# Kernel tuning notes

Measured on AMD Instinct MI355X. Metric: run time of the kernel, lower is better.

## Reference

```python
import jax, jax.numpy as jnp
import numpy as np

ALPHA = 0.8
TOPK = 9
LOW_BOUND = 0.0
EPS = 1e-10
IOU_EPS = 1e-6


def pairwise_iou(boxes1, boxes2):
    # boxes1 [N,4], boxes2 [G,4] in x1,y1,x2,y2 -> IoU [N,G] (mmdet BboxOverlaps2D)
    area1 = (boxes1[:, 2] - boxes1[:, 0]) * (boxes1[:, 3] - boxes1[:, 1])  # [N]
    area2 = (boxes2[:, 2] - boxes2[:, 0]) * (boxes2[:, 3] - boxes2[:, 1])  # [G]
    lt = jnp.maximum(boxes1[:, None, :2], boxes2[None, :, :2])  # [N,G,2]
    rb = jnp.minimum(boxes1[:, None, 2:], boxes2[None, :, 2:])  # [N,G,2]
    wh = jnp.clip(rb - lt, 0.0)
    inter = wh[..., 0] * wh[..., 1]  # [N,G]
    union = area1[:, None] + area2[None, :] - inter
    return inter / jnp.maximum(union, IOU_EPS)


def setup_inputs() -> dict:
    key = jax.random.key(0)
    k1, k2, k3, k4, k5, k6, k7 = jax.random.split(key, 7)
    N, G, C = 65536, 256, 80
    IMG = 1024.0
    points = jax.random.uniform(k1, (N, 2), dtype=jnp.float32) * IMG  # (cy, cx)
    p_xy1 = jax.random.uniform(k2, (N, 2), dtype=jnp.float32) * (IMG - 96.0)
    p_wh = jax.random.uniform(k3, (N, 2), dtype=jnp.float32) * 95.0 + 1.0
    bbox_preds = jnp.concatenate([p_xy1, p_xy1 + p_wh], axis=1)  # valid x1y1x2y2
    g_xy1 = jax.random.uniform(k4, (G, 2), dtype=jnp.float32) * (IMG - 256.0)
    g_wh = jax.random.uniform(k5, (G, 2), dtype=jnp.float32) * 255.0 + 1.0
    gt_bboxes = jnp.concatenate([g_xy1, g_xy1 + g_wh], axis=1)
    cls_scores = jax.random.normal(k6, (N, C), dtype=jnp.float32)
    gt_labels = jax.random.randint(k7, (G,), 0, C)
    return {"points": points, "cls_scores": cls_scores, "bbox_preds": bbox_preds,
            "gt_bboxes": gt_bboxes, "gt_labels": gt_labels}


def reference(points, cls_scores, bbox_preds, gt_bboxes, gt_labels):
    num_points = points.shape[0]
    num_gt = gt_bboxes.shape[0]
    overlaps = pairwise_iou(bbox_preds, gt_bboxes)  # [N,G]
    cls_cost = jax.nn.sigmoid(cls_scores[:, gt_labels])  # [N,G]
    overlaps = cls_cost ** (1.0 - ALPHA) * overlaps ** ALPHA
    # top-k points per GT (torch: overlaps.topk(k, dim=0))
    _, topk_idxs = jax.lax.top_k(overlaps.T, TOPK)  # [G,K]
    candidate_idxs = topk_idxs.T  # [K,G]
    cp = jnp.transpose(points[candidate_idxs], (1, 0, 2))  # [G,K,2] (cy,cx)
    # mle_2d_gaussian_2: per-GT MLE Gaussian over candidate points
    miu = cp.mean(axis=1, keepdims=True)  # [G,1,2]
    diff = cp - miu  # [G,K,2]
    sigma = jnp.einsum('gki,gkj->gij', diff, diff) / TOPK  # [G,2,2]
    a, b = sigma[:, 0, 0], sigma[:, 0, 1]
    c, d = sigma[:, 1, 0], sigma[:, 1, 1]
    det = a * d - b * c  # [G]
    inv = jnp.stack([jnp.stack([d, -b], axis=-1),
                     jnp.stack([-c, a], axis=-1)], axis=-2) / (det + EPS)[:, None, None]
    maha = jnp.einsum('gki,gij,gkj->gk', diff, inv, diff)  # [G,K]
    candidate_w = jnp.exp(-0.5 * maha).T  # [K,G]
    # center-inside-gt validity, evaluated only at candidate points
    cy, cx = cp[:, :, 0], cp[:, :, 1]  # [G,K]
    gx1, gy1, gx2, gy2 = (gt_bboxes[:, i][:, None] for i in range(4))  # [G,1]
    valid = ((cx - gx1 > EPS) & (cy - gy1 > EPS) &
             (gx2 - cx > EPS) & (gy2 - cy > EPS)).T  # [K,G]
    wv = candidate_w * valid.astype(candidate_w.dtype)
    # scatter per-GT weights to points, then max over GTs == scatter-max
    w = jnp.zeros((num_points,), dtype=cls_scores.dtype)
    w = w.at[candidate_idxs.reshape(-1)].max(wv.reshape(-1))
    w = jnp.where(w < LOW_BOUND, jnp.zeros_like(w), w)
    return w
```

## Files before the change

### kernel.cpp

```cpp
#include <hip/hip_runtime.h>
#include <hip/hip_bf16.h>
#include <math.h>

#define NPTS   65536
#define NGT    256
#define NCLS   80
#define TOPK   9
#define GSLICE 32
#define NPB    256
#define SCAP   64


__device__ inline unsigned long long pack_key(float L, unsigned idx) {
    unsigned u   = __float_as_uint(L);
    unsigned k32 = (u & 0x80000000u) ? ~u : (u | 0x80000000u);
    return ((unsigned long long)k32 << 32) | (unsigned)(~idx);
}

__global__ void zero_kernel(float* __restrict__ w, unsigned* __restrict__ cnt) {
    int i = blockIdx.x * 256 + threadIdx.x;
    if (i < NPTS) w[i] = 0.0f;
    if (i < NGT)  cnt[i] = 0u;
}

__global__ __launch_bounds__(256) void filter_kernel(
    const float* __restrict__ cls,
    const float* __restrict__ preds,
    const float* __restrict__ gtb,
    const int*   __restrict__ glab,
    unsigned*    __restrict__ cnt,
    unsigned long long* __restrict__ bucket,
    int cap)
{
    __shared__ float4   gbox[GSLICE];
    __shared__ int      glabs[GSLICE];
    __shared__ float    garea[GSLICE];
    __shared__ unsigned lcnt[GSLICE];
    __shared__ unsigned gbase[GSLICE];
    __shared__ unsigned long long stage[GSLICE][SCAP];

    const int t  = threadIdx.x;
    const int pt = blockIdx.x * NPB + t;
    const int g0 = blockIdx.y * GSLICE;

    if (t < GSLICE) {
        float4 g4 = ((const float4*)gtb)[g0 + t];
        gbox[t]  = g4;
        glabs[t] = glab[g0 + t];
        garea[t] = (g4.z - g4.x) * (g4.w - g4.y);
        lcnt[t]  = 0u;
    }
    float4 pb = ((const float4*)preds)[pt];
    float parea = (pb.z - pb.x) * (pb.w - pb.y);
    __syncthreads();

    const float E1 = 1.0f - 0.8f;

    for (int gi = 0; gi < GSLICE; ++gi) {
        float4 g4 = gbox[gi];
        float ix1 = fmaxf(pb.x, g4.x), iy1 = fmaxf(pb.y, g4.y);
        float ix2 = fminf(pb.z, g4.z), iy2 = fminf(pb.w, g4.w);
        float iw  = fmaxf(ix2 - ix1, 0.0f);
        float ih  = fmaxf(iy2 - iy1, 0.0f);
        float inter = iw * ih;
        if (inter > 0.0f) {
            float uni = fmaxf(parea + garea[gi] - inter, 1e-6f);
            float iou = inter / uni;
            float x = cls[(size_t)pt * NCLS + glabs[gi]];
            float s = 1.0f / (1.0f + expf(-x));
            float L = E1 * log2f(s) + 0.8f * log2f(iou);
            unsigned long long key = pack_key(L, (unsigned)pt);

            unsigned slot = atomicAdd(&lcnt[gi], 1u);
            if (slot < SCAP) {
                stage[gi][slot] = key;
            } else {
                unsigned pos = atomicAdd(&cnt[g0 + gi], 1u);
                if (pos < (unsigned)cap)
                    bucket[(size_t)(g0 + gi) * cap + pos] = key;
            }
        }
    }
    __syncthreads();

    if (t < GSLICE) {
        unsigned c = lcnt[t];
        if (c > SCAP) c = SCAP;
        lcnt[t]  = c;
        gbase[t] = atomicAdd(&cnt[g0 + t], c);
    }
    __syncthreads();

    for (int i = t; i < GSLICE * SCAP; i += 256) {
        int gi = i >> 6;
        int sl = i & (SCAP - 1);
        if (sl < (int)lcnt[gi]) {
            unsigned pos = gbase[gi] + (unsigned)sl;
            if (pos < (unsigned)cap)
                bucket[(size_t)(g0 + gi) * cap + pos] = stage[gi][sl];
        }
    }
}

__global__ __launch_bounds__(256) void select_kernel(
    const unsigned*           __restrict__ cnt,
    const unsigned long long* __restrict__ bucket,
    const float* __restrict__ pts,
    const float* __restrict__ gtb,
    float* __restrict__ w,
    int cap)
{
    const int g    = blockIdx.x;
    const int t    = threadIdx.x;
    const int lane = t & 63;
    const int wid  = t >> 6;

    __shared__ unsigned long long wl[4][TOPK];
    __shared__ unsigned tidx[TOPK];
    __shared__ float ppy[TOPK], ppx[TOPK];

    int n = (int)cnt[g];
    if (n > cap) n = cap;

    unsigned long long loc[TOPK];
#pragma unroll
    for (int k = 0; k < TOPK; ++k) loc[k] = 0ULL;
    if (t < TOPK) loc[0] = pack_key(-INFINITY, (unsigned)t);

    const unsigned long long* src = bucket + (size_t)g * cap;
    for (int i = t; i < n; i += 256) {
        unsigned long long v = src[i];
        if (v > loc[TOPK - 1]) {
            loc[TOPK - 1] = v;
#pragma unroll
            for (int j = TOPK - 1; j > 0; --j) {
                if (loc[j] > loc[j - 1]) {
                    unsigned long long tmp = loc[j];
                    loc[j] = loc[j - 1]; loc[j - 1] = tmp;
                }
            }
        }
    }
#pragma unroll
    for (int a = 0; a < TOPK; ++a)
#pragma unroll
        for (int j = TOPK - 1; j > 0; --j)
            if (loc[j] > loc[j - 1]) {
                unsigned long long tmp = loc[j];
                loc[j] = loc[j - 1]; loc[j - 1] = tmp;
            }

#pragma unroll
    for (int lvl = 0; lvl < 6; ++lvl) {
        const int off = 1 << lvl;
        unsigned long long oth[TOPK];
#pragma unroll
        for (int k = 0; k < TOPK; ++k) oth[k] = __shfl_xor(loc[k], off);
#pragma unroll
        for (int k = 0; k < TOPK; ++k) {
            unsigned long long v = oth[k];
            if (v > loc[TOPK - 1]) {
                loc[TOPK - 1] = v;
#pragma unroll
                for (int j = TOPK - 1; j > 0; --j) {
                    if (loc[j] > loc[j - 1]) {
                        unsigned long long tmp = loc[j];
                        loc[j] = loc[j - 1]; loc[j - 1] = tmp;
                    }
                }
            }
        }
    }

    if (lane == 0) {
#pragma unroll
        for (int k = 0; k < TOPK; ++k) wl[wid][k] = loc[k];
    }
    __syncthreads();

    if (t == 0) {
#pragma unroll
        for (int wv = 1; wv < 4; ++wv) {
#pragma unroll
            for (int k = 0; k < TOPK; ++k) {
                unsigned long long v = wl[wv][k];
                if (v > loc[TOPK - 1]) {
                    loc[TOPK - 1] = v;
#pragma unroll
                    for (int j = TOPK - 1; j > 0; --j) {
                        if (loc[j] > loc[j - 1]) {
                            unsigned long long tmp = loc[j];
                            loc[j] = loc[j - 1]; loc[j - 1] = tmp;
                        }
                    }
                }
            }
        }
#pragma unroll
        for (int k = 0; k < TOPK; ++k)
            tidx[k] = ~(unsigned)(loc[k] & 0xFFFFFFFFu);
    }
    __syncthreads();

    if (t < TOPK) {
        unsigned pi = tidx[t];
        ppy[t] = pts[2 * (size_t)pi];
        ppx[t] = pts[2 * (size_t)pi + 1];
    }
    __syncthreads();

    if (t == 0) {
        float4 g4 = ((const float4*)gtb)[g];
        float m0 = 0.0f, m1 = 0.0f;
#pragma unroll
        for (int k = 0; k < TOPK; ++k) { m0 += ppy[k]; m1 += ppx[k]; }
        m0 /= (float)TOPK; m1 /= (float)TOPK;

        float d0[TOPK], d1[TOPK];
        float a = 0.0f, bb = 0.0f, dd = 0.0f;
#pragma unroll
        for (int k = 0; k < TOPK; ++k) {
            d0[k] = ppy[k] - m0;
            d1[k] = ppx[k] - m1;
            a  += d0[k] * d0[k];
            bb += d0[k] * d1[k];
            dd += d1[k] * d1[k];
        }
        a /= (float)TOPK; bb /= (float)TOPK; dd /= (float)TOPK;
        float det  = a * dd - bb * bb;
        float rinv = 1.0f / (det + 1e-10f);

#pragma unroll
        for (int k = 0; k < TOPK; ++k) {
            float q = d0[k] * (dd * d0[k] - bb * d1[k])
                    + d1[k] * (a  * d1[k] - bb * d0[k]);
            float maha = q * rinv;
            float wt = expf(-0.5f * maha);
            bool valid = (ppx[k] - g4.x > 1e-10f) && (ppy[k] - g4.y > 1e-10f) &&
                         (g4.z - ppx[k] > 1e-10f) && (g4.w - ppy[k] > 1e-10f);
            float wv = valid ? wt : 0.0f;
            atomicMax((int*)&w[tidx[k]], __float_as_int(wv));
        }
    }
}

extern "C" void kernel_launch(void* const* d_in, const int* in_sizes, int n_in,
                              void* d_out, int out_size, void* d_ws, size_t ws_size,
                              hipStream_t stream) {
    const float* points  = (const float*)d_in[0];
    const float* cls     = (const float*)d_in[1];
    const float* preds   = (const float*)d_in[2];
    const float* gtb     = (const float*)d_in[3];
    const int*   glab    = (const int*)d_in[4];
    float* w = (float*)d_out;

    unsigned*           cnt    = (unsigned*)d_ws;
    unsigned long long* bucket = (unsigned long long*)((char*)d_ws + 1024);

    long long avail = ((long long)ws_size - 1024) / (NGT * (long long)sizeof(unsigned long long));
    int cap = (avail < 8192) ? (int)avail : 8192;

    zero_kernel<<<(NPTS + 255) / 256, 256, 0, stream>>>(w, cnt);
    filter_kernel<<<dim3(NPTS / NPB, NGT / GSLICE), 256, 0, stream>>>(
        cls, preds, gtb, glab, cnt, bucket, cap);
    select_kernel<<<NGT, 256, 0, stream>>>(cnt, bucket, points, gtb, w, cap);
}
```

Before: 134.1 us.

## Defer class-score gather and log scoring to select kernel; aggregate shared atomics per wave

```diff
diff --git a/kernel.cpp b/kernel.cpp
--- a/kernel.cpp
+++ b/kernel.cpp
@@ -10,7 +10,6 @@
 #define NPB    256
 #define SCAP   64
 
-
 __device__ inline unsigned long long pack_key(float L, unsigned idx) {
     unsigned u   = __float_as_uint(L);
     unsigned k32 = (u & 0x80000000u) ? ~u : (u | 0x80000000u);
@@ -24,37 +23,32 @@
 }
 
 __global__ __launch_bounds__(256) void filter_kernel(
-    const float* __restrict__ cls,
     const float* __restrict__ preds,
     const float* __restrict__ gtb,
-    const int*   __restrict__ glab,
     unsigned*    __restrict__ cnt,
     unsigned long long* __restrict__ bucket,
     int cap)
 {
     __shared__ float4   gbox[GSLICE];
-    __shared__ int      glabs[GSLICE];
     __shared__ float    garea[GSLICE];
     __shared__ unsigned lcnt[GSLICE];
     __shared__ unsigned gbase[GSLICE];
     __shared__ unsigned long long stage[GSLICE][SCAP];
 
-    const int t  = threadIdx.x;
-    const int pt = blockIdx.x * NPB + t;
-    const int g0 = blockIdx.y * GSLICE;
+    const int t    = threadIdx.x;
+    const int lane = t & 63;
+    const int pt   = blockIdx.x * NPB + t;
+    const int g0   = blockIdx.y * GSLICE;
 
     if (t < GSLICE) {
         float4 g4 = ((const float4*)gtb)[g0 + t];
         gbox[t]  = g4;
-        glabs[t] = glab[g0 + t];
         garea[t] = (g4.z - g4.x) * (g4.w - g4.y);
         lcnt[t]  = 0u;
     }
     float4 pb = ((const float4*)preds)[pt];
     float parea = (pb.z - pb.x) * (pb.w - pb.y);
     __syncthreads();
-
-    const float E1 = 1.0f - 0.8f;
 
     for (int gi = 0; gi < GSLICE; ++gi) {
         float4 g4 = gbox[gi];
@@ -63,21 +57,28 @@
         float iw  = fmaxf(ix2 - ix1, 0.0f);
         float ih  = fmaxf(iy2 - iy1, 0.0f);
         float inter = iw * ih;
-        if (inter > 0.0f) {
+        bool act = inter > 0.0f;
+        unsigned long long mask = __ballot(act);
+        if (act) {
             float uni = fmaxf(parea + garea[gi] - inter, 1e-6f);
             float iou = inter / uni;
-            float x = cls[(size_t)pt * NCLS + glabs[gi]];
-            float s = 1.0f / (1.0f + expf(-x));
-            float L = E1 * log2f(s) + 0.8f * log2f(iou);
-            unsigned long long key = pack_key(L, (unsigned)pt);
-
-            unsigned slot = atomicAdd(&lcnt[gi], 1u);
+            unsigned long long entry =
+                ((unsigned long long)__float_as_uint(iou) << 32) |
+                (unsigned)(~(unsigned)pt);
+
+            int rank   = __popcll(mask & ((1ULL << lane) - 1ULL));
+            int nact   = __popcll(mask);
+            int leader = __ffsll((unsigned long long)mask) - 1;
+            unsigned base = 0;
+            if (lane == leader) base = atomicAdd(&lcnt[gi], (unsigned)nact);
+            base = (unsigned)__shfl((int)base, leader);
+            unsigned slot = base + (unsigned)rank;
             if (slot < SCAP) {
-                stage[gi][slot] = key;
+                stage[gi][slot] = entry;
             } else {
                 unsigned pos = atomicAdd(&cnt[g0 + gi], 1u);
                 if (pos < (unsigned)cap)
-                    bucket[(size_t)(g0 + gi) * cap + pos] = key;
+                    bucket[(size_t)(g0 + gi) * cap + pos] = entry;
             }
         }
     }
@@ -105,6 +106,8 @@
 __global__ __launch_bounds__(256) void select_kernel(
     const unsigned*           __restrict__ cnt,
     const unsigned long long* __restrict__ bucket,
+    const float* __restrict__ cls,
+    const int*   __restrict__ glab,
     const float* __restrict__ pts,
     const float* __restrict__ gtb,
     float* __restrict__ w,
@@ -121,6 +124,8 @@
 
     int n = (int)cnt[g];
     if (n > cap) n = cap;
+    const int lab = glab[g];
+    const float E1 = 1.0f - 0.8f;
 
     unsigned long long loc[TOPK];
 #pragma unroll
@@ -128,17 +133,57 @@
     if (t < TOPK) loc[0] = pack_key(-INFINITY, (unsigned)t);
 
     const unsigned long long* src = bucket + (size_t)g * cap;
-    for (int i = t; i < n; i += 256) {
+
+    int i = t;
+    for (; i + 3 * 256 < n; i += 4 * 256) {
+        unsigned long long v[4];
+        float x[4];
+#pragma unroll
+        for (int j = 0; j < 4; ++j) v[j] = src[i + j * 256];
+#pragma unroll
+        for (int j = 0; j < 4; ++j) {
+            unsigned p = ~(unsigned)(v[j] & 0xFFFFFFFFu);
+            x[j] = cls[(size_t)p * NCLS + lab];
+        }
+#pragma unroll
+        for (int j = 0; j < 4; ++j) {
+            float iou = __uint_as_float((unsigned)(v[j] >> 32));
+            float s   = 1.0f / (1.0f + expf(-x[j]));
+            float L   = E1 * log2f(s) + 0.8f * log2f(iou);
+            unsigned u   = __float_as_uint(L);
+            unsigned k32 = (u & 0x80000000u) ? ~u : (u | 0x80000000u);
+            unsigned long long key =
+                ((unsigned long long)k32 << 32) | (v[j] & 0xFFFFFFFFu);
+            if (key > loc[TOPK - 1]) {
+                loc[TOPK - 1] = key;
+#pragma unroll
+                for (int jj = TOPK - 1; jj > 0; --jj)
+                    if (loc[jj] > loc[jj - 1]) {
+                        unsigned long long tmp = loc[jj];
+                        loc[jj] = loc[jj - 1]; loc[jj - 1] = tmp;
+                    }
+            }
+        }
+    }
+    for (; i < n; i += 256) {
         unsigned long long v = src[i];
-        if (v > loc[TOPK - 1]) {
-            loc[TOPK - 1] = v;
-#pragma unroll
-            for (int j = TOPK - 1; j > 0; --j) {
-                if (loc[j] > loc[j - 1]) {
-                    unsigned long long tmp = loc[j];
-                    loc[j] = loc[j - 1]; loc[j - 1] = tmp;
+        unsigned p = ~(unsigned)(v & 0xFFFFFFFFu);
+        float x   = cls[(size_t)p * NCLS + lab];
+        float iou = __uint_as_float((unsigned)(v >> 32));
+        float s   = 1.0f / (1.0f + expf(-x));
+        float L   = E1 * log2f(s) + 0.8f * log2f(iou);
+        unsigned u   = __float_as_uint(L);
+        unsigned k32 = (u & 0x80000000u) ? ~u : (u | 0x80000000u);
+        unsigned long long key =
+            ((unsigned long long)k32 << 32) | (v & 0xFFFFFFFFu);
+        if (key > loc[TOPK - 1]) {
+            loc[TOPK - 1] = key;
+#pragma unroll
+            for (int jj = TOPK - 1; jj > 0; --jj)
+                if (loc[jj] > loc[jj - 1]) {
+                    unsigned long long tmp = loc[jj];
+                    loc[jj] = loc[jj - 1]; loc[jj - 1] = tmp;
                 }
-            }
         }
     }
 #pragma unroll
@@ -262,6 +307,6 @@
 
     zero_kernel<<<(NPTS + 255) / 256, 256, 0, stream>>>(w, cnt);
     filter_kernel<<<dim3(NPTS / NPB, NGT / GSLICE), 256, 0, stream>>>(
-        cls, preds, gtb, glab, cnt, bucket, cap);
-    select_kernel<<<NGT, 256, 0, stream>>>(cnt, bucket, points, gtb, w, cap);
-}
+        preds, gtb, cnt, bucket, cap);
+    select_kernel<<<NGT, 256, 0, stream>>>(cnt, bucket, cls, glab, points, gtb, w, cap);
+}
```

New measurement: 133.4 us. No clear change (-0.6%).
